# Kernel tuning notes

Measured on AMD Instinct MI355X. Metric: run time of the kernel, lower is better.

## Reference

```python
import jax, jax.numpy as jnp
from jax import lax
import numpy as np

N = 227328   # B(32) * T(64) * 111 ROIs, block-diagonal collated graph
E = 1000000  # thresholded sparse edges
H = 128      # hidden_dim
NB = 111     # brain ROIs per graph (hardcoded in source)
P = 40       # |perm| (pooled node subset)
MAXLEN = 10  # max_path_length
NSTART = 5   # top-5 start nodes


def setup_inputs() -> dict:
    key = jax.random.key(0)
    ks = jax.random.split(key, 12)
    s = 1.0 / np.sqrt(H)
    return dict(
        v=jax.random.normal(ks[0], (N, H), jnp.float32),
        edge_row=jax.random.randint(ks[1], (E,), 0, N, jnp.int32),
        edge_col=jax.random.randint(ks[2], (E,), 0, N, jnp.int32),
        W1=jax.random.normal(ks[3], (H, H), jnp.float32) * s,
        b1=jnp.zeros((H,), jnp.float32),
        g1=jnp.ones((H,), jnp.float32),
        be1=jnp.zeros((H,), jnp.float32),
        W2=jax.random.normal(ks[4], (H, H), jnp.float32) * s,
        b2=jnp.zeros((H,), jnp.float32),
        g2=jnp.ones((H,), jnp.float32),
        be2=jnp.zeros((H,), jnp.float32),
        epsilon=jnp.zeros((1, 1), jnp.float32),
        adj111=jax.random.randint(ks[5], (NB, NB), 0, 2, jnp.int32),
        node_scores=jax.random.normal(ks[6], (NB,), jnp.float32),
        node_feats=jax.random.normal(ks[7], (NB, H), jnp.float32),
        perm=jnp.arange(P, dtype=jnp.int32),
        x_small=jax.random.normal(ks[8], (P, H), jnp.float32),
    )


def _batchnorm(x, g, b, eps=1e-5):
    # BatchNorm1d in training mode: biased batch statistics over node dim
    m = x.mean(0)
    var = x.var(0)
    return g * (x - m) * lax.rsqrt(var + eps) + b


def _gin(v, row, col, epsilon, W1, b1, g1, be1, W2, b2, g2, be2):
    # torch.sparse.mm(a, v): agg[i] = sum_{j: a[i,j]=1} v[j]
    agg = jax.ops.segment_sum(v[col], row, num_segments=v.shape[0])
    h = agg + epsilon[0, 0] * v
    h = jax.nn.relu(_batchnorm(h @ W1 + b1, g1, be1))
    h = jax.nn.relu(_batchnorm(h @ W2 + b2, g2, be2))
    return h


def _biased_random_walk(adj, scores, x, feats, perm):
    soft = jax.nn.softmax(scores)
    order = jnp.argsort(-scores)              # nodes by descending score
    in_perm = jnp.isin(order, perm)
    pos = jnp.where(in_perm, jnp.arange(NB), NB)
    starts = order[jnp.argsort(pos)[:NSTART]]  # first 5 sorted nodes in perm
    start_ok = jnp.arange(NSTART) < jnp.minimum(jnp.sum(in_perm), NSTART)

    def walk_one(carry, se):
        all_visited, xc = carry
        start, ok = se
        skip = jnp.logical_or(~ok, all_visited[start])
        visited0 = all_visited.at[start].set(True)

        def step(c, _):
            cur, visited, alive = c
            nbr = (adj[cur] > 0) & (~visited)
            has = jnp.any(nbr) & alive
            nxt = jnp.argmax(jnp.where(nbr, soft, -jnp.inf))  # greedy by softmax score
            cur2 = jnp.where(has, nxt, cur)
            visited2 = jnp.where(has, visited.at[nxt].set(True), visited)
            return (cur2, visited2, has), (cur2, has)

        (_, visited_f, _), (pn, pv) = lax.scan(
            step, (start, visited0, True), None, length=MAXLEN - 1)
        path = jnp.concatenate([start[None], pn])           # [MAXLEN]
        valid = jnp.concatenate([jnp.array([True]), pv])
        w = jax.nn.softmax(jnp.where(valid, scores[path], -jnp.inf))
        fused = jnp.sum(w[:, None] * feats[path], axis=0)   # [H]
        idx = jnp.argmax(perm == start)
        do = (~skip) & jnp.any(perm == start)
        x_new = jnp.where(do, xc.at[idx].add(fused), xc)
        av_new = jnp.where(skip, all_visited, visited_f)
        return (av_new, x_new), None

    (_, x_out), _ = lax.scan(
        walk_one, (jnp.zeros((NB,), bool), x), (starts, start_ok))
    return x_out


def reference(v, edge_row, edge_col, W1, b1, g1, be1, W2, b2, g2, be2,
              epsilon, adj111, node_scores, node_feats, perm, x_small):
    gin_out = _gin(v, edge_row, edge_col, epsilon,
                   W1, b1, g1, be1, W2, b2, g2, be2)
    x_fused = _biased_random_walk(adj111, node_scores, x_small,
                                  node_feats, perm)
    return gin_out, x_fused
```

## Files before the change

kernel.cpp:

```cpp
#include <hip/hip_runtime.h>
#include <hip/hip_bf16.h>
#include <math.h>

#define N_NODES 227328
#define H_DIM 128
#define NB_ 111
#define P_ 40
#define MAXLEN_ 10
#define NSTART_ 5
#define NH (N_NODES * H_DIM)
#define SCAN_BLK 1024

typedef __attribute__((ext_vector_type(8))) short short8;
typedef __attribute__((ext_vector_type(8))) unsigned short ushort8;
typedef __attribute__((ext_vector_type(4))) float f32x4;


__global__ __launch_bounds__(256) void k_zero(float* wsf, int* cnt, int n) {
    int gstride = gridDim.x * blockDim.x;
    for (int i = blockIdx.x * blockDim.x + threadIdx.x; i < n; i += gstride) cnt[i] = 0;
    if (blockIdx.x == 0)
        for (int i = threadIdx.x; i < 1280; i += 256) wsf[i] = 0.f;
}


__device__ inline unsigned short f2bf(float x) {
    unsigned u = __float_as_uint(x);
    return (unsigned short)((u + 0x7FFFu + ((u >> 16) & 1u)) >> 16);
}

__global__ __launch_bounds__(256) void k_hist_conv(const int* __restrict__ erow, int* cnt, int E,
                                                   const float4* __restrict__ v4,
                                                   ushort8* __restrict__ vb8, int n8) {
    int stride = gridDim.x * blockDim.x;
    int tid = blockIdx.x * blockDim.x + threadIdx.x;
    for (int i = tid; i < n8; i += stride) {
        float4 a = v4[i * 2], b = v4[i * 2 + 1];
        ushort8 o;
        o[0] = f2bf(a.x); o[1] = f2bf(a.y); o[2] = f2bf(a.z); o[3] = f2bf(a.w);
        o[4] = f2bf(b.x); o[5] = f2bf(b.y); o[6] = f2bf(b.z); o[7] = f2bf(b.w);
        vb8[i] = o;
    }
    for (int e = tid; e < E; e += stride)
        atomicAdd(&cnt[erow[e]], 1);
}


__global__ __launch_bounds__(256) void k_scan1(const int* __restrict__ cnt, int* __restrict__ ptr,
                                               int* __restrict__ bsum, int n) {
    __shared__ int s_warp[4];
    int t = threadIdx.x;
    int base = blockIdx.x * SCAN_BLK + t * 4;
    int x0 = (base + 0 < n) ? cnt[base + 0] : 0;
    int x1 = (base + 1 < n) ? cnt[base + 1] : 0;
    int x2 = (base + 2 < n) ? cnt[base + 2] : 0;
    int x3 = (base + 3 < n) ? cnt[base + 3] : 0;
    int tsum = x0 + x1 + x2 + x3;
    int lane = t & 63, w = t >> 6;
    int v = tsum;
#pragma unroll
    for (int m = 1; m < 64; m <<= 1) {
        int o = __shfl_up(v, m, 64);
        if (lane >= m) v += o;
    }
    if (lane == 63) s_warp[w] = v;
    __syncthreads();
    int wadd = 0;
    for (int j = 0; j < w; j++) wadd += s_warp[j];
    int excl = v - tsum + wadd;
    if (base + 0 < n) ptr[base + 0] = excl;
    if (base + 1 < n) ptr[base + 1] = excl + x0;
    if (base + 2 < n) ptr[base + 2] = excl + x0 + x1;
    if (base + 3 < n) ptr[base + 3] = excl + x0 + x1 + x2;
    if (t == 0) bsum[blockIdx.x] = s_warp[0] + s_warp[1] + s_warp[2] + s_warp[3];
}

__global__ __launch_bounds__(256) void k_scan2(int* bsum, int nb) {
    __shared__ int s[256];
    int t = threadIdx.x;
    s[t] = (t < nb) ? bsum[t] : 0;
    __syncthreads();
    if (t == 0) {
        int acc = 0;
        for (int i = 0; i < nb; i++) { int x = s[i]; s[i] = acc; acc += x; }
    }
    __syncthreads();
    if (t < nb) bsum[t] = s[t];
}

__global__ __launch_bounds__(256) void k_scan3(int* __restrict__ ptr, const int* __restrict__ bsum,
                                               int* __restrict__ cur, int n, int E) {
    int stride = gridDim.x * blockDim.x;
    for (int i = blockIdx.x * blockDim.x + threadIdx.x; i < n; i += stride) {
        int p = ptr[i] + bsum[i / SCAN_BLK];
        ptr[i] = p;
        cur[i] = p;
    }
    if (blockIdx.x == 0 && threadIdx.x == 0) ptr[n] = E;
}

__global__ __launch_bounds__(256) void k_fill(const int* __restrict__ erow,
                                              const int* __restrict__ ecol,
                                              int* cur, int* __restrict__ col, int E) {
    int stride = gridDim.x * blockDim.x;
    for (int e = blockIdx.x * blockDim.x + threadIdx.x; e < E; e += stride) {
        int p = atomicAdd(&cur[erow[e]], 1);
        col[p] = ecol[e];
    }
}


__device__ inline float blo(unsigned u) { return __uint_as_float(u << 16); }
__device__ inline float bhi(unsigned u) { return __uint_as_float(u & 0xFFFF0000u); }

__global__ __launch_bounds__(256) void k_agg_bf16(const float* __restrict__ v,
                                                  const unsigned* __restrict__ vbu,
                                                  const int* __restrict__ ptr,
                                                  const int* __restrict__ col,
                                                  const float* __restrict__ epsp,
                                                  float* __restrict__ out, int n) {
    int r = (blockIdx.x * 256 + threadIdx.x) >> 6;
    int lane = threadIdx.x & 63;
    if (r >= n) return;
    float eps = epsp[0];
    float2 a = *((const float2*)(v + (size_t)r * H_DIM) + lane);
    float acx = eps * a.x, acy = eps * a.y;
    int s = ptr[r], e = ptr[r + 1];
    int i = s;
    for (; i + 8 <= e; i += 8) {
        unsigned u0 = vbu[(size_t)col[i + 0] * 64 + lane];
        unsigned u1 = vbu[(size_t)col[i + 1] * 64 + lane];
        unsigned u2 = vbu[(size_t)col[i + 2] * 64 + lane];
        unsigned u3 = vbu[(size_t)col[i + 3] * 64 + lane];
        unsigned u4 = vbu[(size_t)col[i + 4] * 64 + lane];
        unsigned u5 = vbu[(size_t)col[i + 5] * 64 + lane];
        unsigned u6 = vbu[(size_t)col[i + 6] * 64 + lane];
        unsigned u7 = vbu[(size_t)col[i + 7] * 64 + lane];
        acx += ((blo(u0) + blo(u1)) + (blo(u2) + blo(u3))) +
               ((blo(u4) + blo(u5)) + (blo(u6) + blo(u7)));
        acy += ((bhi(u0) + bhi(u1)) + (bhi(u2) + bhi(u3))) +
               ((bhi(u4) + bhi(u5)) + (bhi(u6) + bhi(u7)));
    }
    for (; i + 4 <= e; i += 4) {
        unsigned u0 = vbu[(size_t)col[i + 0] * 64 + lane];
        unsigned u1 = vbu[(size_t)col[i + 1] * 64 + lane];
        unsigned u2 = vbu[(size_t)col[i + 2] * 64 + lane];
        unsigned u3 = vbu[(size_t)col[i + 3] * 64 + lane];
        acx += (blo(u0) + blo(u1)) + (blo(u2) + blo(u3));
        acy += (bhi(u0) + bhi(u1)) + (bhi(u2) + bhi(u3));
    }
    for (; i < e; i++) {
        unsigned u = vbu[(size_t)col[i] * 64 + lane];
        acx += blo(u);
        acy += bhi(u);
    }
    *((float2*)(out + (size_t)r * H_DIM) + lane) = make_float2(acx, acy);
}

__global__ __launch_bounds__(256) void k_agg(const float* __restrict__ v,
                                             const int* __restrict__ ptr,
                                             const int* __restrict__ col,
                                             const float* __restrict__ epsp,
                                             float* __restrict__ out, int n) {
    int r = (blockIdx.x * 256 + threadIdx.x) >> 6;
    int lane = threadIdx.x & 63;
    if (r >= n) return;
    float eps = epsp[0];
    float2 a = *((const float2*)(v + (size_t)r * H_DIM) + lane);
    float acx = eps * a.x, acy = eps * a.y;
    int s = ptr[r], e = ptr[r + 1];
    int i = s;
    for (; i + 4 <= e; i += 4) {
        int c0 = col[i], c1 = col[i + 1], c2 = col[i + 2], c3 = col[i + 3];
        float2 b0 = *((const float2*)(v + (size_t)c0 * H_DIM) + lane);
        float2 b1 = *((const float2*)(v + (size_t)c1 * H_DIM) + lane);
        float2 b2 = *((const float2*)(v + (size_t)c2 * H_DIM) + lane);
        float2 b3 = *((const float2*)(v + (size_t)c3 * H_DIM) + lane);
        acx += (b0.x + b1.x) + (b2.x + b3.x);
        acy += (b0.y + b1.y) + (b2.y + b3.y);
    }
    for (; i < e; i++) {
        int c = col[i];
        float2 b = *((const float2*)(v + (size_t)c * H_DIM) + lane);
        acx += b.x;
        acy += b.y;
    }
    *((float2*)(out + (size_t)r * H_DIM) + lane) = make_float2(acx, acy);
}


__global__ __launch_bounds__(256) void k_init(const float4* __restrict__ v4,
                                              const float* __restrict__ epsp,
                                              float4* __restrict__ out4, int n4) {
    float eps = epsp[0];
    int stride = gridDim.x * blockDim.x;
    for (int i = blockIdx.x * blockDim.x + threadIdx.x; i < n4; i += stride) {
        float4 a = v4[i];
        out4[i] = make_float4(eps * a.x, eps * a.y, eps * a.z, eps * a.w);
    }
}

__global__ __launch_bounds__(256) void k_scatter(const float* __restrict__ v,
                                                 const int* __restrict__ erow,
                                                 const int* __restrict__ ecol,
                                                 float* agg, int E) {
    int tid = blockIdx.x * blockDim.x + threadIdx.x;
    int lane = tid & 63;
    int wave = tid >> 6;
    int nwaves = (gridDim.x * blockDim.x) >> 6;
    for (int e = wave; e < E; e += nwaves) {
        int r = erow[e], c = ecol[e];
        const float2 val = *((const float2*)(v + (size_t)c * H_DIM) + lane);
        float* dst = agg + (size_t)r * H_DIM + lane * 2;
        unsafeAtomicAdd(dst, val.x);
        unsafeAtomicAdd(dst + 1, val.y);
    }
}


__device__ inline void split8(const float* xs, short8& hi, short8& lo) {
#pragma unroll
    for (int e = 0; e < 8; e++) {
        unsigned u = __float_as_uint(xs[e]);
        hi[e] = (short)(unsigned short)(u >> 16);
        float hf = __uint_as_float(u & 0xFFFF0000u);
        lo[e] = (short)(unsigned short)(__float_as_uint(xs[e] - hf) >> 16);
    }
}

template <int BN>
__global__ __launch_bounds__(256, 2) void k_gemm_mfma(
        const float* __restrict__ A, float* __restrict__ C,
        const float* __restrict__ W, const float* __restrict__ bias,
        const float* __restrict__ scl_in, const float* __restrict__ of_in,
        float* __restrict__ sums, float* __restrict__ sumsq) {
    __shared__ unsigned short Whi[128 * 136];
    __shared__ unsigned short Wlo[128 * 136];
    __shared__ float scof[256];
    __shared__ float stats[2][4][128];

    const int t = threadIdx.x;
    const int w = t >> 6;
    const int l = t & 63;
    const int n = l & 15;
    const int g = l >> 4;
    const size_t row0 = (size_t)blockIdx.x * 128 + w * 32;

#pragma unroll 8
    for (int it = 0; it < 64; ++it) {
        int k = it * 2 + (t >> 7);
        int nn = t & 127;
        float wv = W[k * 128 + nn];
        unsigned u = __float_as_uint(wv);
        Whi[nn * 136 + k] = (unsigned short)(u >> 16);
        float hf = __uint_as_float(u & 0xFFFF0000u);
        Wlo[nn * 136 + k] = (unsigned short)(__float_as_uint(wv - hf) >> 16);
    }
    if (BN && t < 128) { scof[t] = scl_in[t]; scof[128 + t] = of_in[t]; }
    __syncthreads();

    float breg[8];
#pragma unroll
    for (int cb = 0; cb < 8; cb++) breg[cb] = bias[cb * 16 + n];

    f32x4 acc[2][8];
#pragma unroll
    for (int rf = 0; rf < 2; rf++)
#pragma unroll
        for (int cb = 0; cb < 8; cb++) acc[rf][cb] = (f32x4){0.f, 0.f, 0.f, 0.f};

    const float* Arow0 = A + (row0 + n) * H_DIM;
    const float* Arow1 = A + (row0 + 16 + n) * H_DIM;

#pragma unroll
    for (int kb = 0; kb < 4; kb++) {
        const int k0 = kb * 32 + g * 8;
        float4 x00 = *(const float4*)(Arow0 + k0);
        float4 x01 = *(const float4*)(Arow0 + k0 + 4);
        float4 x10 = *(const float4*)(Arow1 + k0);
        float4 x11 = *(const float4*)(Arow1 + k0 + 4);
        float xs0[8] = {x00.x, x00.y, x00.z, x00.w, x01.x, x01.y, x01.z, x01.w};
        float xs1[8] = {x10.x, x10.y, x10.z, x10.w, x11.x, x11.y, x11.z, x11.w};
        if (BN) {
            float sc[8], of[8];
            float4 sa = *(const float4*)(scof + k0);
            float4 sb = *(const float4*)(scof + k0 + 4);
            float4 oa = *(const float4*)(scof + 128 + k0);
            float4 ob = *(const float4*)(scof + 128 + k0 + 4);
            sc[0] = sa.x; sc[1] = sa.y; sc[2] = sa.z; sc[3] = sa.w;
            sc[4] = sb.x; sc[5] = sb.y; sc[6] = sb.z; sc[7] = sb.w;
            of[0] = oa.x; of[1] = oa.y; of[2] = oa.z; of[3] = oa.w;
            of[4] = ob.x; of[5] = ob.y; of[6] = ob.z; of[7] = ob.w;
#pragma unroll
            for (int e = 0; e < 8; e++) {
                xs0[e] = fmaxf(fmaf(xs0[e], sc[e], of[e]), 0.f);
                xs1[e] = fmaxf(fmaf(xs1[e], sc[e], of[e]), 0.f);
            }
        }
        short8 ah0, al0, ah1, al1;
        split8(xs0, ah0, al0);
        split8(xs1, ah1, al1);

        short8 wh[8], wl[8];
        const int wb = n * 136 + kb * 32 + g * 8;
#pragma unroll
        for (int cb = 0; cb < 8; cb++) {
            wh[cb] = *(const short8*)(Whi + cb * 2176 + wb);
            wl[cb] = *(const short8*)(Wlo + cb * 2176 + wb);
        }
#pragma unroll
        for (int cb = 0; cb < 8; cb++) {
            acc[0][cb] = __builtin_amdgcn_mfma_f32_16x16x32_bf16(ah0, wh[cb], acc[0][cb], 0, 0, 0);
            acc[1][cb] = __builtin_amdgcn_mfma_f32_16x16x32_bf16(ah1, wh[cb], acc[1][cb], 0, 0, 0);
            acc[0][cb] = __builtin_amdgcn_mfma_f32_16x16x32_bf16(al0, wh[cb], acc[0][cb], 0, 0, 0);
            acc[1][cb] = __builtin_amdgcn_mfma_f32_16x16x32_bf16(al1, wh[cb], acc[1][cb], 0, 0, 0);
            acc[0][cb] = __builtin_amdgcn_mfma_f32_16x16x32_bf16(ah0, wl[cb], acc[0][cb], 0, 0, 0);
            acc[1][cb] = __builtin_amdgcn_mfma_f32_16x16x32_bf16(ah1, wl[cb], acc[1][cb], 0, 0, 0);
        }
    }

    float s[8], s2[8];
#pragma unroll
    for (int cb = 0; cb < 8; cb++) { s[cb] = 0.f; s2[cb] = 0.f; }
#pragma unroll
    for (int cb = 0; cb < 8; cb++) {
        const int c = cb * 16 + n;
#pragma unroll
        for (int rf = 0; rf < 2; rf++) {
            f32x4 o = acc[rf][cb];
            const size_t rbase = (row0 + rf * 16 + g * 4) * H_DIM + c;
#pragma unroll
            for (int r = 0; r < 4; r++) {
                float val = o[r] + breg[cb];
                C[rbase + (size_t)r * H_DIM] = val;
                s[cb] += val;
                s2[cb] += val * val;
            }
        }
    }
#pragma unroll
    for (int cb = 0; cb < 8; cb++) {
        s[cb] += __shfl_xor(s[cb], 16, 64);
        s[cb] += __shfl_xor(s[cb], 32, 64);
        s2[cb] += __shfl_xor(s2[cb], 16, 64);
        s2[cb] += __shfl_xor(s2[cb], 32, 64);
    }
    if (g == 0) {
#pragma unroll
        for (int cb = 0; cb < 8; cb++) {
            stats[0][w][cb * 16 + n] = s[cb];
            stats[1][w][cb * 16 + n] = s2[cb];
        }
    }
    __syncthreads();
    if (t < 128) {
        float S  = stats[0][0][t] + stats[0][1][t] + stats[0][2][t] + stats[0][3][t];
        float S2 = stats[1][0][t] + stats[1][1][t] + stats[1][2][t] + stats[1][3][t];
        unsafeAtomicAdd(sums + t, S);
        unsafeAtomicAdd(sumsq + t, S2);
    }
}

__global__ void k_finalize(const float* __restrict__ sums, const float* __restrict__ sumsq,
                           float* __restrict__ mean, float* __restrict__ scl,
                           float* __restrict__ of,
                           const float* __restrict__ g, const float* __restrict__ beta,
                           float invN) {
    int t = threadIdx.x;
    if (t < H_DIM) {
        float m = sums[t] * invN;
        float var = sumsq[t] * invN - m * m;
        float sc = g[t] * rsqrtf(var + 1e-5f);
        mean[t] = m;
        scl[t] = sc;
        of[t] = beta[t] - m * sc;
    }
}


__device__ inline float block_max4(float v, int t, float* s_r) {
#pragma unroll
    for (int m = 1; m < 64; m <<= 1) v = fmaxf(v, __shfl_xor(v, m, 64));
    if ((t & 63) == 0) s_r[t >> 6] = v;
    __syncthreads();
    float r = fmaxf(fmaxf(s_r[0], s_r[1]), fmaxf(s_r[2], s_r[3]));
    __syncthreads();
    return r;
}

__device__ inline float block_sum4(float v, int t, float* s_r) {
#pragma unroll
    for (int m = 1; m < 64; m <<= 1) v += __shfl_xor(v, m, 64);
    if ((t & 63) == 0) s_r[t >> 6] = v;
    __syncthreads();
    float r = (s_r[0] + s_r[1]) + (s_r[2] + s_r[3]);
    __syncthreads();
    return r;
}

__device__ inline void block_argmax4(float v, int idx, int t, float* s_rv, int* s_ri,
                                     float* outv, int* outi) {
#pragma unroll
    for (int m = 1; m < 64; m <<= 1) {
        float ov = __shfl_xor(v, m, 64);
        int oi = __shfl_xor(idx, m, 64);
        if (ov > v || (ov == v && oi < idx)) { v = ov; idx = oi; }
    }
    if ((t & 63) == 0) { s_rv[t >> 6] = v; s_ri[t >> 6] = idx; }
    __syncthreads();
    float bv = s_rv[0];
    int bi = s_ri[0];
#pragma unroll
    for (int j = 1; j < 4; j++) {
        float ov = s_rv[j];
        int oi = s_ri[j];
        if (ov > bv || (ov == bv && oi < bi)) { bv = ov; bi = oi; }
    }
    *outv = bv;
    *outi = bi;
    __syncthreads();
}

__global__ __launch_bounds__(256) void k_bnwalk(
        float4* y4, const float* __restrict__ scl, const float* __restrict__ of, int n4,
        const int* __restrict__ adj, const float* __restrict__ scores,
        const float* __restrict__ feats, const int* __restrict__ perm,
        const float* __restrict__ xs, float* __restrict__ outw) {
    __shared__ unsigned long long s_am0[NB_], s_am1[NB_];
    __shared__ float s_scores[NB_], s_soft[NB_];
    __shared__ int s_perm[P_];
    __shared__ unsigned char s_inperm[NB_], s_sel[NB_], s_allvis[NB_], s_vis[NB_];
    __shared__ int s_starts[NSTART_];
    __shared__ int s_path[MAXLEN_];
    __shared__ unsigned char s_valid[MAXLEN_];
    __shared__ float s_w[MAXLEN_];
    __shared__ int s_cur, s_alive, s_do, s_idx, s_skip;
    __shared__ float s_rv[4];
    __shared__ int s_ri[4];

    const int t = threadIdx.x;

    if (blockIdx.x != 0) {
        int stride = (gridDim.x - 1) * 256;
        for (int i = (blockIdx.x - 1) * 256 + t; i < n4; i += stride) {
            int c = (i & 31) * 4;
            float4 a = y4[i];
            a.x = fmaxf(fmaf(a.x, scl[c + 0], of[c + 0]), 0.f);
            a.y = fmaxf(fmaf(a.y, scl[c + 1], of[c + 1]), 0.f);
            a.z = fmaxf(fmaf(a.z, scl[c + 2], of[c + 2]), 0.f);
            a.w = fmaxf(fmaf(a.w, scl[c + 3], of[c + 3]), 0.f);
            y4[i] = a;
        }
        return;
    }

    for (int i = t; i < P_ * H_DIM; i += 256) outw[i] = xs[i];
    if (t < P_) s_perm[t] = perm[t];
    if (t < NB_) { s_scores[t] = scores[t]; s_allvis[t] = 0; s_sel[t] = 0; }
    if (t < NB_) {
        const int* row = adj + t * NB_;
        unsigned long long m0 = 0ull, m1 = 0ull;
#pragma unroll
        for (int j = 0; j < 64; j++) m0 |= (unsigned long long)(row[j] > 0 ? 1u : 0u) << j;
        for (int j = 64; j < NB_; j++) m1 |= (unsigned long long)(row[j] > 0 ? 1u : 0u) << (j - 64);
        s_am0[t] = m0;
        s_am1[t] = m1;
    }
    __syncthreads();
    if (t < NB_) {
        unsigned char inp = 0;
        for (int j = 0; j < P_; j++) inp |= (s_perm[j] == t) ? 1 : 0;
        s_inperm[t] = inp;
    }
    __syncthreads();

    float myv = (t < NB_) ? s_scores[t] : -INFINITY;
    float mx = block_max4(myv, t, s_rv);
    float e = (t < NB_) ? expf(s_scores[t] - mx) : 0.f;
    float ssum = block_sum4(e, t, s_rv);
    if (t < NB_) s_soft[t] = e / ssum;

    float ninf = block_sum4((t < NB_ && s_inperm[t]) ? 1.f : 0.f, t, s_rv);
    int nin = (int)(ninf + 0.5f);
    int nok = nin < NSTART_ ? nin : NSTART_;
    __syncthreads();

    for (int r = 0; r < NSTART_; r++) {
        bool useIn = (r < nin);
        bool elig = (t < NB_) && !s_sel[t] && (((s_inperm[t] != 0)) == useIn);
        float v = elig ? s_scores[t] : -INFINITY;
        float mv; int mi;
        block_argmax4(v, elig ? t : 0x7fffffff, t, s_rv, s_ri, &mv, &mi);
        if (t == 0) s_starts[r] = mi;
        if (t == mi && t < NB_) s_sel[t] = 1;
        __syncthreads();
    }

    for (int s = 0; s < NSTART_; s++) {
        if (t == 0) {
            int start = s_starts[s];
            int ok = (s < nok) ? 1 : 0;
            int skip = (!ok) || s_allvis[start];
            s_skip = skip;
            s_cur = start;
            s_alive = 1;
            s_path[0] = start;
            s_valid[0] = 1;
            int idx = 0, found = 0;
            for (int j = 0; j < P_; j++)
                if (!found && s_perm[j] == start) { idx = j; found = 1; }
            s_idx = idx;
            s_do = (!skip) && found;
        }
        __syncthreads();
        if (t < NB_) s_vis[t] = s_allvis[t];
        __syncthreads();
        if (t == 0) s_vis[s_cur] = 1;
        __syncthreads();

        for (int st = 1; st < MAXLEN_; st++) {
            int cur = s_cur;
            int alive = s_alive;
            int abit = (t < 64) ? (int)((s_am0[cur] >> t) & 1ull)
                                : (int)((s_am1[cur] >> (t - 64)) & 1ull);
            bool elig = (t < NB_) && alive && abit && (!s_vis[t]);
            float v = elig ? s_soft[t] : -INFINITY;
            float mv; int mi;
            block_argmax4(v, elig ? t : 0x7fffffff, t, s_rv, s_ri, &mv, &mi);
            if (t == 0) {
                int has = (mv > -INFINITY) ? 1 : 0;
                if (has) { s_cur = mi; s_vis[mi] = 1; }
                s_path[st] = has ? mi : cur;
                s_valid[st] = (unsigned char)has;
                s_alive = has;
            }
            __syncthreads();
        }

        if (t == 0) {
            float mxw = -INFINITY;
            for (int st = 0; st < MAXLEN_; st++)
                if (s_valid[st]) mxw = fmaxf(mxw, s_scores[s_path[st]]);
            float sw = 0.f;
            for (int st = 0; st < MAXLEN_; st++) {
                float ev = s_valid[st] ? expf(s_scores[s_path[st]] - mxw) : 0.f;
                s_w[st] = ev; sw += ev;
            }
            float inv = 1.f / sw;
            for (int st = 0; st < MAXLEN_; st++) s_w[st] *= inv;
        }
        __syncthreads();
        if (s_do && t < H_DIM) {
            float acc = 0.f;
            for (int st = 0; st < MAXLEN_; st++)
                acc += s_w[st] * feats[s_path[st] * H_DIM + t];
            outw[s_idx * H_DIM + t] += acc;
        }
        __syncthreads();
        if (!s_skip && t < NB_) s_allvis[t] = s_vis[t];
        __syncthreads();
    }
}


extern "C" void kernel_launch(void* const* d_in, const int* in_sizes, int n_in,
                              void* d_out, int out_size, void* d_ws, size_t ws_size,
                              hipStream_t stream) {
    const float* v    = (const float*)d_in[0];
    const int*   erow = (const int*)d_in[1];
    const int*   ecol = (const int*)d_in[2];
    const float* W1   = (const float*)d_in[3];
    const float* b1   = (const float*)d_in[4];
    const float* g1   = (const float*)d_in[5];
    const float* be1  = (const float*)d_in[6];
    const float* W2   = (const float*)d_in[7];
    const float* b2   = (const float*)d_in[8];
    const float* g2   = (const float*)d_in[9];
    const float* be2  = (const float*)d_in[10];
    const float* epsp = (const float*)d_in[11];
    const int*   adj  = (const int*)d_in[12];
    const float* scr  = (const float*)d_in[13];
    const float* fts  = (const float*)d_in[14];
    const int*   perm = (const int*)d_in[15];
    const float* xs   = (const float*)d_in[16];

    float* out = (float*)d_out;
    float* wsf = (float*)d_ws;
    float* sums1 = wsf,        *sumsq1 = wsf + 128,  *mean1 = wsf + 256,  *scl1 = wsf + 384,  *of1 = wsf + 512;
    float* sums2 = wsf + 640,  *sumsq2 = wsf + 768,  *mean2 = wsf + 896,  *scl2 = wsf + 1024, *of2 = wsf + 1152;

    const int E  = in_sizes[1];
    const int N  = N_NODES;
    const int n4 = NH / 4;

    int* ws_i = (int*)(wsf + 1280);
    int* cnt  = ws_i;
    int* ptr  = ws_i + (N + 1);
    int* cur  = ws_i + 2 * (N + 1);
    int* col  = ws_i + 3 * (N + 1);
    size_t need_csr = 1280 * 4 + (size_t)(3 * (N + 1) + E) * 4;
    size_t off_vb   = (need_csr + 15) & ~(size_t)15;
    size_t need_vb  = off_vb + (size_t)NH * 2;
    unsigned* vbu = (unsigned*)((char*)d_ws + off_vb);

    if (ws_size >= need_csr) {
        const int nb = (N + SCAN_BLK - 1) / SCAN_BLK;
        bool useBf = (ws_size >= need_vb);
        k_zero<<<512, 256, 0, stream>>>(wsf, cnt, N + 1);
        if (useBf)
            k_hist_conv<<<2048, 256, 0, stream>>>(erow, cnt, E, (const float4*)v,
                                                  (ushort8*)vbu, NH / 8);
        else
            k_hist_conv<<<2048, 256, 0, stream>>>(erow, cnt, E, (const float4*)v,
                                                  (ushort8*)vbu, 0);
        k_scan1<<<nb, 256, 0, stream>>>(cnt, ptr, cur , N);
        k_scan2<<<1, 256, 0, stream>>>(cur, nb);
        k_scan3<<<512, 256, 0, stream>>>(ptr, cur, cnt , N, E);
        k_fill<<<1024, 256, 0, stream>>>(erow, ecol, cnt, col, E);
        if (useBf)
            k_agg_bf16<<<N / 4, 256, 0, stream>>>(v, vbu, ptr, col, epsp, out, N);
        else
            k_agg<<<N / 4, 256, 0, stream>>>(v, ptr, col, epsp, out, N);
    } else {
        k_zero<<<512, 256, 0, stream>>>(wsf, cnt, 0);
        k_init<<<2048, 256, 0, stream>>>((const float4*)v, epsp, (float4*)out, n4);
        k_scatter<<<4096, 256, 0, stream>>>(v, erow, ecol, out, E);
    }

    k_gemm_mfma<0><<<N / 128, 256, 0, stream>>>(out, out, W1, b1, nullptr, nullptr,
                                                sums1, sumsq1);
    k_finalize<<<1, 128, 0, stream>>>(sums1, sumsq1, mean1, scl1, of1, g1, be1, 1.f / N);
    k_gemm_mfma<1><<<N / 128, 256, 0, stream>>>(out, out, W2, b2, scl1, of1,
                                                sums2, sumsq2);
    k_finalize<<<1, 128, 0, stream>>>(sums2, sumsq2, mean2, scl2, of2, g2, be2, 1.f / N);
    k_bnwalk<<<2049, 256, 0, stream>>>((float4*)out, scl2, of2, n4,
                                       adj, scr, fts, perm, xs, out + NH);
}
```

Measured before the change: 675.0 us.

## Fold BN finalize into consumers and run random walk in a single wavefront

```diff
diff --git a/kernel.cpp b/kernel.cpp
--- a/kernel.cpp
+++ b/kernel.cpp
@@ -232,7 +232,8 @@
 __global__ __launch_bounds__(256, 2) void k_gemm_mfma(
         const float* __restrict__ A, float* __restrict__ C,
         const float* __restrict__ W, const float* __restrict__ bias,
-        const float* __restrict__ scl_in, const float* __restrict__ of_in,
+        const float* __restrict__ bn_sums, const float* __restrict__ bn_sumsq,
+        const float* __restrict__ bn_g, const float* __restrict__ bn_be, float invN,
         float* __restrict__ sums, float* __restrict__ sumsq) {
     __shared__ unsigned short Whi[128 * 136];
     __shared__ unsigned short Wlo[128 * 136];
@@ -256,7 +257,13 @@
         float hf = __uint_as_float(u & 0xFFFF0000u);
         Wlo[nn * 136 + k] = (unsigned short)(__float_as_uint(wv - hf) >> 16);
     }
-    if (BN && t < 128) { scof[t] = scl_in[t]; scof[128 + t] = of_in[t]; }
+    if (BN && t < 128) {
+        float m = bn_sums[t] * invN;
+        float var = bn_sumsq[t] * invN - m * m;
+        float s = bn_g[t] * rsqrtf(var + 1e-5f);
+        scof[t] = s;
+        scof[128 + t] = bn_be[t] - m * s;
+    }
     __syncthreads();
 
     float breg[8];
@@ -361,204 +368,188 @@
     }
 }
 
-__global__ void k_finalize(const float* __restrict__ sums, const float* __restrict__ sumsq,
-                           float* __restrict__ mean, float* __restrict__ scl,
-                           float* __restrict__ of,
-                           const float* __restrict__ g, const float* __restrict__ beta,
-                           float invN) {
-    int t = threadIdx.x;
-    if (t < H_DIM) {
-        float m = sums[t] * invN;
-        float var = sumsq[t] * invN - m * m;
-        float sc = g[t] * rsqrtf(var + 1e-5f);
-        mean[t] = m;
-        scl[t] = sc;
-        of[t] = beta[t] - m * sc;
-    }
-}
-
-
-__device__ inline float block_max4(float v, int t, float* s_r) {
+
+__device__ inline float wave_max_f(float v) {
 #pragma unroll
     for (int m = 1; m < 64; m <<= 1) v = fmaxf(v, __shfl_xor(v, m, 64));
-    if ((t & 63) == 0) s_r[t >> 6] = v;
-    __syncthreads();
-    float r = fmaxf(fmaxf(s_r[0], s_r[1]), fmaxf(s_r[2], s_r[3]));
-    __syncthreads();
-    return r;
-}
-
-__device__ inline float block_sum4(float v, int t, float* s_r) {
+    return v;
+}
+
+__device__ inline float wave_sum_f(float v) {
 #pragma unroll
     for (int m = 1; m < 64; m <<= 1) v += __shfl_xor(v, m, 64);
-    if ((t & 63) == 0) s_r[t >> 6] = v;
-    __syncthreads();
-    float r = (s_r[0] + s_r[1]) + (s_r[2] + s_r[3]);
-    __syncthreads();
-    return r;
-}
-
-__device__ inline void block_argmax4(float v, int idx, int t, float* s_rv, int* s_ri,
-                                     float* outv, int* outi) {
+    return v;
+}
+
+__device__ inline void wave_argmax(float v, int idx, float* ov, int* oi) {
 #pragma unroll
     for (int m = 1; m < 64; m <<= 1) {
-        float ov = __shfl_xor(v, m, 64);
-        int oi = __shfl_xor(idx, m, 64);
-        if (ov > v || (ov == v && oi < idx)) { v = ov; idx = oi; }
-    }
-    if ((t & 63) == 0) { s_rv[t >> 6] = v; s_ri[t >> 6] = idx; }
-    __syncthreads();
-    float bv = s_rv[0];
-    int bi = s_ri[0];
-#pragma unroll
-    for (int j = 1; j < 4; j++) {
-        float ov = s_rv[j];
-        int oi = s_ri[j];
-        if (ov > bv || (ov == bv && oi < bi)) { bv = ov; bi = oi; }
-    }
-    *outv = bv;
-    *outi = bi;
-    __syncthreads();
+        float nv = __shfl_xor(v, m, 64);
+        int ni = __shfl_xor(idx, m, 64);
+        if (nv > v || (nv == v && ni < idx)) { v = nv; idx = ni; }
+    }
+    *ov = v; *oi = idx;
 }
 
 __global__ __launch_bounds__(256) void k_bnwalk(
-        float4* y4, const float* __restrict__ scl, const float* __restrict__ of, int n4,
+        float4* y4, const float* __restrict__ bn_sums, const float* __restrict__ bn_sumsq,
+        const float* __restrict__ bn_g, const float* __restrict__ bn_be, float invN, int n4,
         const int* __restrict__ adj, const float* __restrict__ scores,
         const float* __restrict__ feats, const int* __restrict__ perm,
         const float* __restrict__ xs, float* __restrict__ outw) {
-    __shared__ unsigned long long s_am0[NB_], s_am1[NB_];
-    __shared__ float s_scores[NB_], s_soft[NB_];
-    __shared__ int s_perm[P_];
-    __shared__ unsigned char s_inperm[NB_], s_sel[NB_], s_allvis[NB_], s_vis[NB_];
-    __shared__ int s_starts[NSTART_];
-    __shared__ int s_path[MAXLEN_];
-    __shared__ unsigned char s_valid[MAXLEN_];
-    __shared__ float s_w[MAXLEN_];
-    __shared__ int s_cur, s_alive, s_do, s_idx, s_skip;
-    __shared__ float s_rv[4];
-    __shared__ int s_ri[4];
-
     const int t = threadIdx.x;
 
     if (blockIdx.x != 0) {
+        int i0 = (blockIdx.x - 1) * 256 + t;
+        int c = (i0 & 31) * 4;
+        float sc[4], of[4];
+#pragma unroll
+        for (int j = 0; j < 4; j++) {
+            float m = bn_sums[c + j] * invN;
+            float var = bn_sumsq[c + j] * invN - m * m;
+            float s = bn_g[c + j] * rsqrtf(var + 1e-5f);
+            sc[j] = s;
+            of[j] = bn_be[c + j] - m * s;
+        }
         int stride = (gridDim.x - 1) * 256;
-        for (int i = (blockIdx.x - 1) * 256 + t; i < n4; i += stride) {
-            int c = (i & 31) * 4;
+        for (int i = i0; i < n4; i += stride) {
             float4 a = y4[i];
-            a.x = fmaxf(fmaf(a.x, scl[c + 0], of[c + 0]), 0.f);
-            a.y = fmaxf(fmaf(a.y, scl[c + 1], of[c + 1]), 0.f);
-            a.z = fmaxf(fmaf(a.z, scl[c + 2], of[c + 2]), 0.f);
-            a.w = fmaxf(fmaf(a.w, scl[c + 3], of[c + 3]), 0.f);
+            a.x = fmaxf(fmaf(a.x, sc[0], of[0]), 0.f);
+            a.y = fmaxf(fmaf(a.y, sc[1], of[1]), 0.f);
+            a.z = fmaxf(fmaf(a.z, sc[2], of[2]), 0.f);
+            a.w = fmaxf(fmaf(a.w, sc[3], of[3]), 0.f);
             y4[i] = a;
         }
         return;
     }
-
-    for (int i = t; i < P_ * H_DIM; i += 256) outw[i] = xs[i];
-    if (t < P_) s_perm[t] = perm[t];
-    if (t < NB_) { s_scores[t] = scores[t]; s_allvis[t] = 0; s_sel[t] = 0; }
-    if (t < NB_) {
-        const int* row = adj + t * NB_;
-        unsigned long long m0 = 0ull, m1 = 0ull;
-#pragma unroll
-        for (int j = 0; j < 64; j++) m0 |= (unsigned long long)(row[j] > 0 ? 1u : 0u) << j;
-        for (int j = 64; j < NB_; j++) m1 |= (unsigned long long)(row[j] > 0 ? 1u : 0u) << (j - 64);
-        s_am0[t] = m0;
-        s_am1[t] = m1;
-    }
-    __syncthreads();
-    if (t < NB_) {
-        unsigned char inp = 0;
-        for (int j = 0; j < P_; j++) inp |= (s_perm[j] == t) ? 1 : 0;
-        s_inperm[t] = inp;
-    }
-    __syncthreads();
-
-    float myv = (t < NB_) ? s_scores[t] : -INFINITY;
-    float mx = block_max4(myv, t, s_rv);
-    float e = (t < NB_) ? expf(s_scores[t] - mx) : 0.f;
-    float ssum = block_sum4(e, t, s_rv);
-    if (t < NB_) s_soft[t] = e / ssum;
-
-    float ninf = block_sum4((t < NB_ && s_inperm[t]) ? 1.f : 0.f, t, s_rv);
-    int nin = (int)(ninf + 0.5f);
+    if (t >= 64) return;
+
+    const int l = t;
+    const bool h0 = l < NB_;
+    const bool h1 = (l + 64) < NB_;
+    float sc0f = h0 ? scores[l] : -INFINITY;
+    float sc1f = h1 ? scores[l + 64] : -INFINITY;
+
+    unsigned long long am0s0 = 0, am1s0 = 0, am0s1 = 0, am1s1 = 0;
+    for (int r = 0; r < NB_; r++) {
+        int a0 = h0 ? adj[r * NB_ + l] : 0;
+        int a1 = h1 ? adj[r * NB_ + l + 64] : 0;
+        unsigned long long b0 = __ballot(a0 > 0);
+        unsigned long long b1 = __ballot(a1 > 0);
+        if (r < 64) {
+            if (l == r) { am0s0 = b0; am1s0 = b1; }
+        } else {
+            if (l == r - 64) { am0s1 = b0; am1s1 = b1; }
+        }
+    }
+
+    float smax = wave_max_f(fmaxf(sc0f, sc1f));
+    float e0 = h0 ? expf(sc0f - smax) : 0.f;
+    float e1 = h1 ? expf(sc1f - smax) : 0.f;
+    float ssum = wave_sum_f(e0 + e1);
+    float soft0 = e0 / ssum, soft1 = e1 / ssum;
+
+    bool in0 = false, in1 = false;
+    for (int j = 0; j < P_; j++) {
+        int p = perm[j];
+        in0 |= (p == l);
+        in1 |= (p == l + 64);
+    }
+    int nin = __popcll(__ballot(in0 && h0)) + __popcll(__ballot(in1 && h1));
     int nok = nin < NSTART_ ? nin : NSTART_;
-    __syncthreads();
-
+
+    unsigned long long sel0 = 0, sel1 = 0;
+    int starts[NSTART_];
+#pragma unroll
     for (int r = 0; r < NSTART_; r++) {
         bool useIn = (r < nin);
-        bool elig = (t < NB_) && !s_sel[t] && (((s_inperm[t] != 0)) == useIn);
-        float v = elig ? s_scores[t] : -INFINITY;
+        bool eb0 = h0 && !((sel0 >> l) & 1ull) && (in0 == useIn);
+        bool eb1 = h1 && !((sel1 >> l) & 1ull) && (in1 == useIn);
+        float v0 = eb0 ? sc0f : -INFINITY;
+        float v1 = eb1 ? sc1f : -INFINITY;
+        float v; int idx;
+        if (v1 > v0) { v = v1; idx = l + 64; } else { v = v0; idx = l; }
         float mv; int mi;
-        block_argmax4(v, elig ? t : 0x7fffffff, t, s_rv, s_ri, &mv, &mi);
-        if (t == 0) s_starts[r] = mi;
-        if (t == mi && t < NB_) s_sel[t] = 1;
-        __syncthreads();
-    }
-
+        wave_argmax(v, idx, &mv, &mi);
+        starts[r] = mi;
+        if (mi < 64) sel0 |= 1ull << mi; else sel1 |= 1ull << (mi - 64);
+    }
+
+    for (int i = l; i < P_ * H_DIM / 4; i += 64)
+        ((float4*)outw)[i] = ((const float4*)xs)[i];
+
+    unsigned long long av0 = 0, av1 = 0;
+#pragma unroll
     for (int s = 0; s < NSTART_; s++) {
-        if (t == 0) {
-            int start = s_starts[s];
-            int ok = (s < nok) ? 1 : 0;
-            int skip = (!ok) || s_allvis[start];
-            s_skip = skip;
-            s_cur = start;
-            s_alive = 1;
-            s_path[0] = start;
-            s_valid[0] = 1;
-            int idx = 0, found = 0;
-            for (int j = 0; j < P_; j++)
-                if (!found && s_perm[j] == start) { idx = j; found = 1; }
-            s_idx = idx;
-            s_do = (!skip) && found;
-        }
-        __syncthreads();
-        if (t < NB_) s_vis[t] = s_allvis[t];
-        __syncthreads();
-        if (t == 0) s_vis[s_cur] = 1;
-        __syncthreads();
-
+        int start = starts[s];
+        bool ok = (s < nok);
+        bool avs = (start < 64) ? ((av0 >> start) & 1ull) : ((av1 >> (start - 64)) & 1ull);
+        bool skip = (!ok) || avs;
+        unsigned long long vis0 = av0, vis1 = av1;
+        if (start < 64) vis0 |= 1ull << start; else vis1 |= 1ull << (start - 64);
+        int cur = start;
+        bool alive = true;
+        int path[MAXLEN_];
+        bool pv[MAXLEN_];
+        path[0] = start; pv[0] = true;
+#pragma unroll
         for (int st = 1; st < MAXLEN_; st++) {
-            int cur = s_cur;
-            int alive = s_alive;
-            int abit = (t < 64) ? (int)((s_am0[cur] >> t) & 1ull)
-                                : (int)((s_am1[cur] >> (t - 64)) & 1ull);
-            bool elig = (t < NB_) && alive && abit && (!s_vis[t]);
-            float v = elig ? s_soft[t] : -INFINITY;
+            unsigned long long m0, m1;
+            if (cur < 64) { m0 = __shfl(am0s0, cur, 64); m1 = __shfl(am1s0, cur, 64); }
+            else          { m0 = __shfl(am0s1, cur - 64, 64); m1 = __shfl(am1s1, cur - 64, 64); }
+            bool eb0 = alive && h0 && ((m0 >> l) & 1ull) && !((vis0 >> l) & 1ull);
+            bool eb1 = alive && h1 && ((m1 >> l) & 1ull) && !((vis1 >> l) & 1ull);
+            float v0 = eb0 ? soft0 : -INFINITY;
+            float v1 = eb1 ? soft1 : -INFINITY;
+            float v; int idx;
+            if (v1 > v0) { v = v1; idx = l + 64; } else { v = v0; idx = l; }
             float mv; int mi;
-            block_argmax4(v, elig ? t : 0x7fffffff, t, s_rv, s_ri, &mv, &mi);
-            if (t == 0) {
-                int has = (mv > -INFINITY) ? 1 : 0;
-                if (has) { s_cur = mi; s_vis[mi] = 1; }
-                s_path[st] = has ? mi : cur;
-                s_valid[st] = (unsigned char)has;
-                s_alive = has;
+            wave_argmax(v, idx, &mv, &mi);
+            bool hasn = (mv > -INFINITY);
+            if (hasn) {
+                cur = mi;
+                if (mi < 64) vis0 |= 1ull << mi; else vis1 |= 1ull << (mi - 64);
             }
-            __syncthreads();
-        }
-
-        if (t == 0) {
-            float mxw = -INFINITY;
-            for (int st = 0; st < MAXLEN_; st++)
-                if (s_valid[st]) mxw = fmaxf(mxw, s_scores[s_path[st]]);
-            float sw = 0.f;
+            path[st] = cur;
+            pv[st] = hasn;
+            alive = hasn;
+        }
+        float stsc[MAXLEN_];
+#pragma unroll
+        for (int st = 0; st < MAXLEN_; st++) {
+            int pn = path[st];
+            stsc[st] = (pn < 64) ? __shfl(sc0f, pn, 64) : __shfl(sc1f, pn - 64, 64);
+        }
+        float mxw = -INFINITY;
+#pragma unroll
+        for (int st = 0; st < MAXLEN_; st++)
+            if (pv[st]) mxw = fmaxf(mxw, stsc[st]);
+        float wv[MAXLEN_];
+        float sw = 0.f;
+#pragma unroll
+        for (int st = 0; st < MAXLEN_; st++) {
+            float ev = pv[st] ? expf(stsc[st] - mxw) : 0.f;
+            wv[st] = ev; sw += ev;
+        }
+        float winv = 1.f / sw;
+        int fidx = 0; bool found = false;
+        for (int j = 0; j < P_; j++) {
+            int p = perm[j];
+            if (!found && p == start) { fidx = j; found = true; }
+        }
+        bool dow = (!skip) && found;
+        if (dow) {
+            float a0 = 0.f, a1 = 0.f;
+#pragma unroll
             for (int st = 0; st < MAXLEN_; st++) {
-                float ev = s_valid[st] ? expf(s_scores[s_path[st]] - mxw) : 0.f;
-                s_w[st] = ev; sw += ev;
+                const float* fr = feats + path[st] * H_DIM;
+                a0 += wv[st] * fr[l];
+                a1 += wv[st] * fr[l + 64];
             }
-            float inv = 1.f / sw;
-            for (int st = 0; st < MAXLEN_; st++) s_w[st] *= inv;
-        }
-        __syncthreads();
-        if (s_do && t < H_DIM) {
-            float acc = 0.f;
-            for (int st = 0; st < MAXLEN_; st++)
-                acc += s_w[st] * feats[s_path[st] * H_DIM + t];
-            outw[s_idx * H_DIM + t] += acc;
-        }
-        __syncthreads();
-        if (!s_skip && t < NB_) s_allvis[t] = s_vis[t];
-        __syncthreads();
+            outw[fidx * H_DIM + l] += a0 * winv;
+            outw[fidx * H_DIM + l + 64] += a1 * winv;
+        }
+        if (!skip) { av0 = vis0; av1 = vis1; }
     }
 }
 
@@ -586,12 +577,13 @@
 
     float* out = (float*)d_out;
     float* wsf = (float*)d_ws;
-    float* sums1 = wsf,        *sumsq1 = wsf + 128,  *mean1 = wsf + 256,  *scl1 = wsf + 384,  *of1 = wsf + 512;
-    float* sums2 = wsf + 640,  *sumsq2 = wsf + 768,  *mean2 = wsf + 896,  *scl2 = wsf + 1024, *of2 = wsf + 1152;
+    float* sums1 = wsf,       *sumsq1 = wsf + 128;
+    float* sums2 = wsf + 256, *sumsq2 = wsf + 384;
 
     const int E  = in_sizes[1];
     const int N  = N_NODES;
     const int n4 = NH / 4;
+    const float invN = 1.f / N;
 
     int* ws_i = (int*)(wsf + 1280);
     int* cnt  = ws_i;
@@ -627,12 +619,12 @@
         k_scatter<<<4096, 256, 0, stream>>>(v, erow, ecol, out, E);
     }
 
-    k_gemm_mfma<0><<<N / 128, 256, 0, stream>>>(out, out, W1, b1, nullptr, nullptr,
+    k_gemm_mfma<0><<<N / 128, 256, 0, stream>>>(out, out, W1, b1,
+                                                nullptr, nullptr, nullptr, nullptr, 0.f,
                                                 sums1, sumsq1);
-    k_finalize<<<1, 128, 0, stream>>>(sums1, sumsq1, mean1, scl1, of1, g1, be1, 1.f / N);
-    k_gemm_mfma<1><<<N / 128, 256, 0, stream>>>(out, out, W2, b2, scl1, of1,
+    k_gemm_mfma<1><<<N / 128, 256, 0, stream>>>(out, out, W2, b2,
+                                                sums1, sumsq1, g1, be1, invN,
                                                 sums2, sumsq2);
-    k_finalize<<<1, 128, 0, stream>>>(sums2, sumsq2, mean2, scl2, of2, g2, be2, 1.f / N);
-    k_bnwalk<<<2049, 256, 0, stream>>>((float4*)out, scl2, of2, n4,
+    k_bnwalk<<<2049, 256, 0, stream>>>((float4*)out, sums2, sumsq2, g2, be2, invN, n4,
                                        adj, scr, fts, perm, xs, out + NH);
 }
```

Result: slower. 851.2 us (+26.1%).
